# Kernel tuning notes

Hardware: AMD Instinct MI355X
Metric: run time of the kernel (lower is better)

Reference implementation:

```python
import jax, jax.numpy as jnp
import numpy as np

N_NODES = 100000
N_EDGES = 1600000
NODE_IN = 6
EDGE_IN = 4
HID = 128


def _glorot(key, shape):
    fan_in, fan_out = shape[0], shape[1]
    lim = (6.0 / (fan_in + fan_out)) ** 0.5
    return jax.random.uniform(key, shape, jnp.float32, -lim, lim)


def setup_inputs() -> dict:
    key = jax.random.key(0)
    ks = jax.random.split(key, 16)
    x = jax.random.normal(ks[0], (N_NODES, NODE_IN), jnp.float32)
    edge_index = jax.random.randint(ks[1], (2, N_EDGES), 0, N_NODES, jnp.int64)
    edge_attr = jax.random.normal(ks[2], (N_EDGES, EDGE_IN), jnp.float32)
    # SAGEConv params: out = x @ W_root + mean_neigh @ W_neigh + b
    params = {
        "w1_root": _glorot(ks[3], (NODE_IN, HID)),
        "w1_neigh": _glorot(ks[4], (NODE_IN, HID)),
        "b1": jnp.zeros((HID,), jnp.float32),
        "w2_root": _glorot(ks[5], (HID, HID)),
        "w2_neigh": _glorot(ks[6], (HID, HID)),
        "b2": jnp.zeros((HID,), jnp.float32),
        "w_e1": _glorot(ks[7], (2 * HID + EDGE_IN, HID)),
        "b_e1": jnp.zeros((HID,), jnp.float32),
        "w_e2": _glorot(ks[8], (HID, HID // 2)),
        "b_e2": jnp.zeros((HID // 2,), jnp.float32),
        "w_e3": _glorot(ks[9], (HID // 2, 1)),
        "b_e3": jnp.zeros((1,), jnp.float32),
    }
    return {"x": x, "edge_index": edge_index, "edge_attr": edge_attr, **params}


def _sage(x, src, dst, w_root, w_neigh, b):
    # mean aggregation of source features into destination nodes
    agg = jax.ops.segment_sum(x[src], dst, num_segments=N_NODES)
    cnt = jax.ops.segment_sum(jnp.ones((src.shape[0], 1), x.dtype), dst, num_segments=N_NODES)
    mean = agg / jnp.maximum(cnt, 1.0)
    return x @ w_root + mean @ w_neigh + b


def reference(x, edge_index, edge_attr,
              w1_root, w1_neigh, b1, w2_root, w2_neigh, b2,
              w_e1, b_e1, w_e2, b_e2, w_e3, b_e3):
    src, dst = edge_index[0], edge_index[1]
    h = jax.nn.relu(_sage(x, src, dst, w1_root, w1_neigh, b1))
    # dropout is identity in eval mode
    h = jax.nn.relu(_sage(h, src, dst, w2_root, w2_neigh, b2))
    # per-edge representation: [h[src], h[dst], edge_attr] -> MLP -> scalar
    e = jnp.concatenate([h[src], h[dst], edge_attr], axis=-1)  # [E, 2H+Ein]
    e = jax.nn.relu(e @ w_e1 + b_e1)
    e = jax.nn.relu(e @ w_e2 + b_e2)
    out = (e @ w_e3 + b_e3).squeeze(-1)  # [E]
    return out
```

## Files before the change

### kernel.cpp

```cpp
#include <hip/hip_runtime.h>
#include <hip/hip_bf16.h>
#include <stdint.h>


typedef unsigned short u16;
typedef short bf16x8 __attribute__((ext_vector_type(8)));
typedef float f32x4 __attribute__((ext_vector_type(4)));
typedef float f32x2 __attribute__((ext_vector_type(2)));

#define NMASK 0x1FFFF

__device__ __forceinline__ u16 f2b(float f) {
  unsigned u = __builtin_bit_cast(unsigned, f);
  u = u + 0x7fffu + ((u >> 16) & 1u);
  return (u16)(u >> 16);
}
__device__ __forceinline__ float bflo(unsigned u) {
  return __builtin_bit_cast(float, u << 16);
}
__device__ __forceinline__ float bfhi(unsigned u) {
  return __builtin_bit_cast(float, u & 0xffff0000u);
}
__device__ __forceinline__ f32x2 unpk2(unsigned u) {
  return (f32x2){bflo(u), bfhi(u)};
}
__device__ __forceinline__ unsigned pack2bf(float a, float b) {
  unsigned ua = __builtin_bit_cast(unsigned, a);
  unsigned ub = __builtin_bit_cast(unsigned, b);
  ua = ua + 0x7fffu + ((ua >> 16) & 1u);
  ub = ub + 0x7fffu + ((ub >> 16) & 1u);
  return (ua >> 16) | (ub & 0xffff0000u);
}
__device__ __forceinline__ unsigned packrn(f32x2 f) {
  __hip_bfloat162 h = __float22bfloat162_rn(make_float2(f.x, f.y));
  unsigned r;
  __builtin_memcpy(&r, &h, 4);
  return r;
}

__global__ void hist_kernel(const int* __restrict__ ei, int* __restrict__ cnt,
                            int E) {
  int e = blockIdx.x * blockDim.x + threadIdx.x;
  if (e < E) atomicAdd(&cnt[ei[E + e]], 1);
}

__global__ void scan_block_sums(const int* __restrict__ cnt,
                                int* __restrict__ partial, int N) {
  __shared__ int red[256];
  int t = threadIdx.x;
  int n = blockIdx.x * 256 + t;
  red[t] = (n < N) ? cnt[n] : 0;
  __syncthreads();
  for (int off = 128; off; off >>= 1) {
    if (t < off) red[t] += red[t + off];
    __syncthreads();
  }
  if (t == 0) partial[blockIdx.x] = red[0];
}

__global__ void scan_partials(int* __restrict__ partial,
                              int* __restrict__ rowptr, int NBLK, int E,
                              int N) {
  __shared__ int sc[512];
  int t = threadIdx.x;
  int v = (t < NBLK) ? partial[t] : 0;
  sc[t] = v;
  __syncthreads();
  for (int off = 1; off < 512; off <<= 1) {
    int a = (t >= off) ? sc[t - off] : 0;
    __syncthreads();
    sc[t] += a;
    __syncthreads();
  }
  if (t < NBLK) partial[t] = sc[t] - v;
  if (t == 0) rowptr[N] = E;
}

__global__ void scan_final(const int* __restrict__ partial,
                           int* __restrict__ cursor, int* __restrict__ rowptr,
                           int N) {
  __shared__ int sc[256];
  int t = threadIdx.x;
  int n = blockIdx.x * 256 + t;
  int v = (n < N) ? cursor[n] : 0;
  sc[t] = v;
  __syncthreads();
  for (int off = 1; off < 256; off <<= 1) {
    int a = (t >= off) ? sc[t - off] : 0;
    __syncthreads();
    sc[t] += a;
    __syncthreads();
  }
  int excl = partial[blockIdx.x] + sc[t] - v;
  if (n < N) {
    rowptr[n] = excl;
    cursor[n] = excl;
  }
}

__global__ void scatter_rec(const int* __restrict__ ei,
                            const float* __restrict__ attr,
                            int* __restrict__ cursor, uint4* __restrict__ rec,
                            unsigned* __restrict__ src4, int E) {
  int e = blockIdx.x * blockDim.x + threadIdx.x;
  if (e >= E) return;
  int s = ei[e];
  int d = ei[E + e];
  float4 a4 = *(const float4*)(attr + (size_t)e * 4);
  int pos = atomicAdd(&cursor[d], 1);
  uint4 r;
  r.x = (unsigned)s | ((unsigned)(d & 0x7FFF) << 17);
  r.y = ((unsigned)d >> 15) | ((unsigned)e << 2);
  r.z = pack2bf(a4.x, a4.y);
  r.w = pack2bf(a4.z, a4.w);
  rec[pos] = r;
  src4[pos] = (unsigned)s;
}

__global__ void pack_weights(const float* __restrict__ w2_root,
                             const float* __restrict__ w2_neigh,
                             const float* __restrict__ w_e1,
                             const float* __restrict__ w_e2,
                             const float* __restrict__ b_e1,
                             u16* __restrict__ B2f, u16* __restrict__ WSDf,
                             u16* __restrict__ W2f, float* __restrict__ pbias) {
  int t = blockIdx.x * 256 + threadIdx.x;
  if (t < 32768) {
    int j = t & 7, lane = (t >> 3) & 63, nt = (t >> 9) & 7, kt = t >> 12;
    int k = kt * 32 + (lane >> 4) * 8 + j;
    int n = nt * 16 + (lane & 15);
    float v = (k < 128) ? w2_root[k * 128 + n] : w2_neigh[(k - 128) * 128 + n];
    B2f[t] = f2b(v);
  } else if (t < 65536) {
    int t2 = t - 32768;
    int j = t2 & 7, lane = (t2 >> 3) & 63, nt = (t2 >> 9) & 15, kt = t2 >> 13;
    int k = kt * 32 + (lane >> 4) * 8 + j;
    int n = nt * 16 + (lane & 15);
    float v = (n < 128) ? w_e1[k * 128 + n] : w_e1[(128 + k) * 128 + (n - 128)];
    WSDf[t2] = f2b(v);
  } else if (t < 73728) {
    int t2 = t - 65536;
    int j = t2 & 7, lane = (t2 >> 3) & 63, nt = (t2 >> 9) & 3, kt = t2 >> 11;
    int k = kt * 32 + (lane >> 4) * 8 + j;
    int n = nt * 16 + (lane & 15);
    W2f[t2] = f2b(w_e2[k * 64 + n]);
  } else if (t < 73984) {
    int n = t - 73728;
    pbias[n] = (n < 128) ? 0.0f : b_e1[n - 128];
  }
}

__global__ __launch_bounds__(256) void agg1_kernel(
    const float* __restrict__ x, const int* __restrict__ rowptr,
    const unsigned* __restrict__ src4, float* __restrict__ mean1, int N) {
  int n = blockIdx.x * 4 + (threadIdx.x >> 6);
  if (n >= N) return;
  int lane = threadIdx.x & 63;
  int g = lane >> 3;
  int c = lane & 7;
  int beg = rowptr[n], end = rowptr[n + 1];
  float a = 0.0f;
  if (c < 6) {
    int idx[4];
#pragma unroll
    for (int j = 0; j < 4; j++) {
      int ii = beg + g + j * 8;
      idx[j] = (ii < end) ? (int)src4[ii] : -1;
    }
    float v[4];
#pragma unroll
    for (int j = 0; j < 4; j++)
      v[j] = x[(size_t)(idx[j] < 0 ? 0 : idx[j]) * 6 + c];
#pragma unroll
    for (int j = 0; j < 4; j++)
      if (idx[j] >= 0) a += v[j];
    for (int ii = beg + g + 32; ii < end; ii += 8) {
      a += x[(size_t)src4[ii] * 6 + c];
    }
  }
  a += __shfl_xor(a, 8, 64);
  a += __shfl_xor(a, 16, 64);
  a += __shfl_xor(a, 32, 64);
  if (g == 0 && c < 6)
    mean1[(size_t)n * 6 + c] = a / (float)max(end - beg, 1);
}

__global__ __launch_bounds__(256) void dense1_kernel(
    const float* __restrict__ x, const float* __restrict__ mean1,
    const float* __restrict__ w_root, const float* __restrict__ w_neigh,
    const float* __restrict__ b, u16* __restrict__ cat2b, int N) {
  __shared__ float sxm[384];
  int t = threadIdx.x;
  int col = t & 127;
  int half = t >> 7;
  float wr[6], wn[6];
#pragma unroll
  for (int j = 0; j < 6; j++) {
    wr[j] = w_root[j * 128 + col];
    wn[j] = w_neigh[j * 128 + col];
  }
  float bb = b[col];
  for (int base = blockIdx.x * 32; base < N; base += gridDim.x * 32) {
    int cnt = min(32, N - base) * 6;
    __syncthreads();
    for (int i = t; i < 384; i += 256) {
      if (i < 192)
        sxm[i] = (i < cnt) ? x[(size_t)base * 6 + i] : 0.0f;
      else
        sxm[i] = (i - 192 < cnt) ? mean1[(size_t)base * 6 + (i - 192)] : 0.0f;
    }
    __syncthreads();
#pragma unroll
    for (int sub = 0; sub < 16; sub++) {
      int nl = sub * 2 + half;
      int n = base + nl;
      if (n < N) {
        float s = bb;
#pragma unroll
        for (int j = 0; j < 6; j++)
          s += sxm[nl * 6 + j] * wr[j] + sxm[192 + nl * 6 + j] * wn[j];
        cat2b[(size_t)n * 256 + col] = f2b(fmaxf(s, 0.0f));
      }
    }
  }
}

__global__ __launch_bounds__(256) void agg2_kernel(
    const u16* __restrict__ cat2b, u16* __restrict__ cat2w,
    const int* __restrict__ rowptr, const unsigned* __restrict__ src4, int N) {
  int n = blockIdx.x * 4 + (threadIdx.x >> 6);
  if (n >= N) return;
  int lane = threadIdx.x & 63;
  int g = lane >> 4;
  int c = lane & 15;
  int beg = rowptr[n], end = rowptr[n + 1];
  f32x2 acc2[4];
#pragma unroll
  for (int j = 0; j < 4; j++) acc2[j] = (f32x2){0.f, 0.f};

  const int DEPTH = 8;
  int idx[DEPTH];
#pragma unroll
  for (int j = 0; j < DEPTH; j++) {
    int ii = beg + g + j * 4;
    idx[j] = (ii < end) ? (int)src4[ii] : -1;
  }
  uint4 u[DEPTH];
#pragma unroll
  for (int j = 0; j < DEPTH; j++) {
    int s = idx[j] < 0 ? 0 : idx[j];
    u[j] = *(const uint4*)(cat2b + (size_t)s * 256 + c * 8);
  }
#pragma unroll
  for (int j = 0; j < DEPTH; j++) {
    if (idx[j] >= 0) {
      acc2[0] += unpk2(u[j].x);
      acc2[1] += unpk2(u[j].y);
      acc2[2] += unpk2(u[j].z);
      acc2[3] += unpk2(u[j].w);
    }
  }
  for (int ii = beg + g + DEPTH * 4; ii < end; ii += 4) {
    uint4 uu = *(const uint4*)(cat2b + (size_t)src4[ii] * 256 + c * 8);
    acc2[0] += unpk2(uu.x);
    acc2[1] += unpk2(uu.y);
    acc2[2] += unpk2(uu.z);
    acc2[3] += unpk2(uu.w);
  }
#pragma unroll
  for (int j = 0; j < 4; j++) {
    acc2[j].x += __shfl_xor(acc2[j].x, 16, 64);
    acc2[j].y += __shfl_xor(acc2[j].y, 16, 64);
    acc2[j].x += __shfl_xor(acc2[j].x, 32, 64);
    acc2[j].y += __shfl_xor(acc2[j].y, 32, 64);
  }
  if (g == 0) {
    float inv = 1.0f / (float)max(end - beg, 1);
    uint4 ov;
    ov.x = packrn(acc2[0] * inv);
    ov.y = packrn(acc2[1] * inv);
    ov.z = packrn(acc2[2] * inv);
    ov.w = packrn(acc2[3] * inv);
    *(uint4*)(cat2w + (size_t)n * 256 + 128 + c * 8) = ov;
  }
}

template <int KT, int NT, bool RELU>
__global__ __launch_bounds__(512) void mfma_gemm(
    const u16* __restrict__ A, int lda, const u16* __restrict__ Bf,
    const float* __restrict__ bias, u16* __restrict__ C, int ldc, int M) {
  __shared__ u16 sB[KT * NT * 512];
  int tid = threadIdx.x;
  for (int i = tid; i < KT * NT * 64; i += 512)
    ((uint4*)sB)[i] = ((const uint4*)Bf)[i];
  int w = tid >> 6, l = tid & 63;
  int quad = l >> 4, col16 = l & 15;
  int rowA = blockIdx.x * 128 + w * 16 + col16;
  bool rv = rowA < M;
  const u16* ap = A + (size_t)rowA * lda + quad * 8;
  f32x4 acc[NT];
#pragma unroll
  for (int nt = 0; nt < NT; nt++) acc[nt] = (f32x4){0.f, 0.f, 0.f, 0.f};
  __syncthreads();
#pragma unroll
  for (int kt = 0; kt < KT; kt++) {
    bf16x8 av = {};
    if (rv) av = *(const bf16x8*)(ap + kt * 32);
#pragma unroll
    for (int nt = 0; nt < NT; nt++) {
      bf16x8 bv = *(const bf16x8*)(sB + ((kt * NT + nt) * 64 + l) * 8);
      acc[nt] = __builtin_amdgcn_mfma_f32_16x16x32_bf16(av, bv, acc[nt], 0, 0, 0);
    }
  }
  int rowbase = blockIdx.x * 128 + w * 16 + quad * 4;
#pragma unroll
  for (int r = 0; r < 4; r++) {
    int row = rowbase + r;
    if (row < M) {
#pragma unroll
      for (int nt = 0; nt < NT; nt++) {
        float v = acc[nt][r] + bias[nt * 16 + col16];
        if (RELU) v = fmaxf(v, 0.0f);
        C[(size_t)row * ldc + nt * 16 + col16] = f2b(v);
      }
    }
  }
}

__global__ __launch_bounds__(256) void edge_mfma_kernel(
    const u16* __restrict__ Pcatb, const uint4* __restrict__ rec,
    const u16* __restrict__ W2f, const float* __restrict__ b_e2,
    const float* __restrict__ w_e3, const float* __restrict__ b_e3,
    const float* __restrict__ w_e1, float* __restrict__ out, int E) {
  __shared__ u16 sV[64 * 136];
  __shared__ u16 sW2[8192];

  int tid = threadIdx.x;
  int w = tid >> 6, l = tid & 63, quad = l >> 4, c16 = l & 15;
  int eg = l >> 4, ac = l & 15;
  u16* sVw = sV + w * 16 * 136;

  for (int i = tid; i < 1024; i += 256)
    ((uint4*)sW2)[i] = ((const uint4*)W2f)[i];
  __syncthreads();

  f32x2 wa2[4][4];
#pragma unroll
  for (int j = 0; j < 4; j++) {
    float4 w0 = *(const float4*)(w_e1 + (256 + j) * 128 + ac * 8);
    float4 w1 = *(const float4*)(w_e1 + (256 + j) * 128 + ac * 8 + 4);
    wa2[j][0] = (f32x2){w0.x, w0.y};
    wa2[j][1] = (f32x2){w0.z, w0.w};
    wa2[j][2] = (f32x2){w1.x, w1.y};
    wa2[j][3] = (f32x2){w1.z, w1.w};
  }
  float w3v[4], be2[4];
#pragma unroll
  for (int nt = 0; nt < 4; nt++) {
    w3v[nt] = w_e3[nt * 16 + c16];
    be2[nt] = b_e2[nt * 16 + c16];
  }
  float b3 = b_e3[0];

  int tiles = (E + 15) >> 4;
  int NW = gridDim.x * 4;
  int t = blockIdx.x * 4 + w;

  uint4 rcA[4], rcB[4];
  uint4 ps[4];

  auto load_rec = [&](int tt, uint4* rcv) {
#pragma unroll
    for (int it = 0; it < 4; it++) {
      int e = min(tt * 16 + it * 4 + eg, E - 1);
      rcv[it] = rec[e];
    }
  };

  auto process = [&](int t, uint4* cur, uint4* nxt) {
    bool hasnext = (t + NW < tiles);
    uint4 pdv[4];
#pragma unroll
    for (int it = 0; it < 4; it++) {
      int d = (int)(((cur[it].x >> 17) | (cur[it].y << 15)) & NMASK);
      pdv[it] = *(const uint4*)(Pcatb + (size_t)d * 256 + 128 + ac * 8);
    }
#pragma unroll
    for (int it = 0; it < 4; it++) {
      int e = it * 4 + eg;
      uint4 psu = ps[it], pdu = pdv[it];
      f32x2 a01 = unpk2(cur[it].z);
      f32x2 a23 = unpk2(cur[it].w);
      unsigned pu[4] = {psu.x, psu.y, psu.z, psu.w};
      unsigned du[4] = {pdu.x, pdu.y, pdu.z, pdu.w};
      uint4 ov;
      unsigned* op = (unsigned*)&ov;
#pragma unroll
      for (int p2 = 0; p2 < 4; p2++) {
        f32x2 f = unpk2(pu[p2]) + unpk2(du[p2]);
        f += a01.x * wa2[0][p2];
        f += a01.y * wa2[1][p2];
        f += a23.x * wa2[2][p2];
        f += a23.y * wa2[3][p2];
        f = __builtin_elementwise_max(f, (f32x2){0.f, 0.f});
        op[p2] = packrn(f);
      }
      *(uint4*)(sVw + e * 136 + ac * 8) = ov;
      if (ac == 0) *(unsigned*)(sVw + e * 136 + 128) = cur[it].y >> 2;
      if (hasnext) {
        int s = (int)(nxt[it].x & NMASK);
        ps[it] = *(const uint4*)(Pcatb + (size_t)s * 256 + ac * 8);
      }
    }
    if (t + 2 * NW < tiles) load_rec(t + 2 * NW, cur);
    f32x4 acc[4];
#pragma unroll
    for (int nt = 0; nt < 4; nt++) acc[nt] = (f32x4){0.f, 0.f, 0.f, 0.f};
    const u16* vp = sVw + c16 * 136 + quad * 8;
#pragma unroll
    for (int kt = 0; kt < 4; kt++) {
      bf16x8 av = *(const bf16x8*)(vp + kt * 32);
#pragma unroll
      for (int nt = 0; nt < 4; nt++) {
        bf16x8 bv = *(const bf16x8*)(sW2 + ((kt * 4 + nt) * 64 + l) * 8);
        acc[nt] =
            __builtin_amdgcn_mfma_f32_16x16x32_bf16(av, bv, acc[nt], 0, 0, 0);
      }
    }
#pragma unroll
    for (int r = 0; r < 4; r++) {
      float p = 0.0f;
#pragma unroll
      for (int nt = 0; nt < 4; nt++)
        p += fmaxf(acc[nt][r] + be2[nt], 0.0f) * w3v[nt];
      p += __shfl_xor(p, 1, 64);
      p += __shfl_xor(p, 2, 64);
      p += __shfl_xor(p, 4, 64);
      p += __shfl_xor(p, 8, 64);
      if (c16 == 0) {
        int eloc = quad * 4 + r;
        if (t * 16 + eloc < E) {
          unsigned eid = *(const unsigned*)(sVw + eloc * 136 + 128);
          out[eid] = p + b3;
        }
      }
    }
  };

  if (t >= tiles) return;
  load_rec(t, rcA);
#pragma unroll
  for (int it = 0; it < 4; it++) {
    int s = (int)(rcA[it].x & NMASK);
    ps[it] = *(const uint4*)(Pcatb + (size_t)s * 256 + ac * 8);
  }
  if (t + NW < tiles) load_rec(t + NW, rcB);

  while (t < tiles) {
    process(t, rcA, rcB);
    t += NW;
    if (t >= tiles) break;
    process(t, rcB, rcA);
    t += NW;
  }
}

extern "C" void kernel_launch(void* const* d_in, const int* in_sizes, int n_in,
                              void* d_out, int out_size, void* d_ws,
                              size_t ws_size, hipStream_t stream) {
  const float* x        = (const float*)d_in[0];
  const int*   ei       = (const int*)d_in[1];
  const float* attr     = (const float*)d_in[2];
  const float* w1_root  = (const float*)d_in[3];
  const float* w1_neigh = (const float*)d_in[4];
  const float* b1       = (const float*)d_in[5];
  const float* w2_root  = (const float*)d_in[6];
  const float* w2_neigh = (const float*)d_in[7];
  const float* b2       = (const float*)d_in[8];
  const float* w_e1     = (const float*)d_in[9];
  const float* b_e1     = (const float*)d_in[10];
  const float* w_e2     = (const float*)d_in[11];
  const float* b_e2     = (const float*)d_in[12];
  const float* w_e3     = (const float*)d_in[13];
  const float* b_e3     = (const float*)d_in[14];
  float* out = (float*)d_out;

  int N = in_sizes[0] / 6;
  int E = in_sizes[2] / 4;
  int NBLK = (N + 255) / 256;

  int* wsi = (int*)d_ws;
  int*      rowptr  = wsi;
  int*      cursor  = wsi + 100004;
  int*      partial = wsi + 200004;
  unsigned* src4    = (unsigned*)(wsi + 200516);
  uint4*    rec     = (uint4*)(wsi + 1800520);
  float*    mean1   = (float*)(wsi + 8200520);
  u16*      cat2b   = (u16*)(wsi + 8800520);
  u16*      h2b     = (u16*)(wsi + 21600520);
  u16*      B2f     = (u16*)(wsi + 28000520);
  u16*      WSDf    = (u16*)(wsi + 28016904);
  u16*      W2f     = (u16*)(wsi + 28033288);
  float*    pbias   = (float*)(wsi + 28037384);

  (void)hipMemsetAsync(cursor, 0, (size_t)N * sizeof(int), stream);

  pack_weights<<<289, 256, 0, stream>>>(w2_root, w2_neigh, w_e1, w_e2, b_e1,
                                        B2f, WSDf, W2f, pbias);

  hist_kernel<<<(E + 255) / 256, 256, 0, stream>>>(ei, cursor, E);
  scan_block_sums<<<NBLK, 256, 0, stream>>>(cursor, partial, N);
  scan_partials<<<1, 512, 0, stream>>>(partial, rowptr, NBLK, E, N);
  scan_final<<<NBLK, 256, 0, stream>>>(partial, cursor, rowptr, N);
  scatter_rec<<<(E + 255) / 256, 256, 0, stream>>>(ei, attr, cursor, rec,
                                                   src4, E);

  agg1_kernel<<<(N + 3) / 4, 256, 0, stream>>>(x, rowptr, src4, mean1, N);
  dense1_kernel<<<1024, 256, 0, stream>>>(x, mean1, w1_root, w1_neigh, b1,
                                          cat2b, N);

  agg2_kernel<<<(N + 3) / 4, 256, 0, stream>>>(cat2b, cat2b, rowptr, src4, N);

  int gblocks = (N + 127) / 128;
  mfma_gemm<8, 8, true><<<gblocks, 512, 0, stream>>>(cat2b, 256, B2f, b2, h2b,
                                                     128, N);
  mfma_gemm<4, 16, false><<<gblocks, 512, 0, stream>>>(h2b, 128, WSDf, pbias,
                                                       cat2b, 256, N);

  edge_mfma_kernel<<<1024, 256, 0, stream>>>(cat2b, rec, W2f, b_e2, w_e3,
                                             b_e3, w_e1, out, E);
}
```

Baseline: 578.5 us.

## Bucket edges by dst/src ranges and pin dst buckets to XCDs

Edge records are no longer stored in dst-CSR order. They are grouped into 8×64 buckets keyed on the dst range and the src range, built with a new shared-memory histogram, a scan and a scatter pass. The edge MLP kernel gives each group of blocks (blockIdx & 7) one dst range, so blocks that likely run on the same XCD gather a bounded slice of node features, and src gathers within a bucket stay local. This aims to raise L2 hit rates for the random node-feature gathers. In exchange it adds three extra passes over the edge list and hardcodes bucket divisors that assume about 100k nodes.

```diff
diff --git a/kernel.cpp b/kernel.cpp
--- a/kernel.cpp
+++ b/kernel.cpp
@@ -9,6 +9,8 @@
 typedef float f32x2 __attribute__((ext_vector_type(2)));
 
 #define NMASK 0x1FFFF
+#define DDIV 12500
+#define SDIV 1563
 
 __device__ __forceinline__ u16 f2b(float f) {
   unsigned u = __builtin_bit_cast(unsigned, f);
@@ -98,23 +100,73 @@
   }
 }
 
-__global__ void scatter_rec(const int* __restrict__ ei,
-                            const float* __restrict__ attr,
-                            int* __restrict__ cursor, uint4* __restrict__ rec,
+__global__ void scatter_src(const int* __restrict__ ei,
+                            int* __restrict__ cursor,
                             unsigned* __restrict__ src4, int E) {
   int e = blockIdx.x * blockDim.x + threadIdx.x;
   if (e >= E) return;
   int s = ei[e];
   int d = ei[E + e];
+  int pos = atomicAdd(&cursor[d], 1);
+  src4[pos] = (unsigned)s;
+}
+
+__global__ void bucket_hist(const int* __restrict__ ei, int* __restrict__ bhist,
+                            int E) {
+  __shared__ int h[512];
+  int t = threadIdx.x;
+  h[t] = 0;
+  h[t + 256] = 0;
+  __syncthreads();
+  int e = blockIdx.x * blockDim.x + t;
+  if (e < E) {
+    int s = ei[e];
+    int d = ei[E + e];
+    int key = (d / DDIV) * 64 + s / SDIV;
+    atomicAdd(&h[key], 1);
+  }
+  __syncthreads();
+  if (h[t]) atomicAdd(&bhist[t], h[t]);
+  if (h[t + 256]) atomicAdd(&bhist[t + 256], h[t + 256]);
+}
+
+__global__ void bucket_scan(const int* __restrict__ bhist,
+                            int* __restrict__ bptr, int* __restrict__ bcur,
+                            int E) {
+  __shared__ int sc[512];
+  int t = threadIdx.x;
+  int v = bhist[t];
+  sc[t] = v;
+  __syncthreads();
+  for (int off = 1; off < 512; off <<= 1) {
+    int a = (t >= off) ? sc[t - off] : 0;
+    __syncthreads();
+    sc[t] += a;
+    __syncthreads();
+  }
+  int excl = sc[t] - v;
+  bptr[t] = excl;
+  bcur[t] = excl;
+  if (t == 0) bptr[512] = E;
+}
+
+__global__ void scatter2_rec(const int* __restrict__ ei,
+                             const float* __restrict__ attr,
+                             int* __restrict__ bcur, uint4* __restrict__ rec,
+                             int E) {
+  int e = blockIdx.x * blockDim.x + threadIdx.x;
+  if (e >= E) return;
+  int s = ei[e];
+  int d = ei[E + e];
   float4 a4 = *(const float4*)(attr + (size_t)e * 4);
-  int pos = atomicAdd(&cursor[d], 1);
+  int key = (d / DDIV) * 64 + s / SDIV;
+  int pos = atomicAdd(&bcur[key], 1);
   uint4 r;
   r.x = (unsigned)s | ((unsigned)(d & 0x7FFF) << 17);
   r.y = ((unsigned)d >> 15) | ((unsigned)e << 2);
   r.z = pack2bf(a4.x, a4.y);
   r.w = pack2bf(a4.z, a4.w);
   rec[pos] = r;
-  src4[pos] = (unsigned)s;
 }
 
 __global__ void pack_weights(const float* __restrict__ w2_root,
@@ -331,7 +383,8 @@
     const u16* __restrict__ Pcatb, const uint4* __restrict__ rec,
     const u16* __restrict__ W2f, const float* __restrict__ b_e2,
     const float* __restrict__ w_e3, const float* __restrict__ b_e3,
-    const float* __restrict__ w_e1, float* __restrict__ out, int E) {
+    const float* __restrict__ w_e1, const int* __restrict__ bptr,
+    float* __restrict__ out, int E) {
   __shared__ u16 sV[64 * 136];
   __shared__ u16 sW2[8192];
 
@@ -362,9 +415,12 @@
   }
   float b3 = b_e3[0];
 
-  int tiles = (E + 15) >> 4;
-  int NW = gridDim.x * 4;
-  int t = blockIdx.x * 4 + w;
+  int s8 = blockIdx.x & 7;
+  int tb = bptr[s8 * 64] >> 4;
+  int te = (bptr[(s8 + 1) * 64] + 15) >> 4;
+  int wi = (blockIdx.x >> 3) * 4 + w;
+  const int NW = 512;
+  int t = tb + wi;
 
   uint4 rcA[4], rcB[4];
   uint4 ps[4];
@@ -378,7 +434,7 @@
   };
 
   auto process = [&](int t, uint4* cur, uint4* nxt) {
-    bool hasnext = (t + NW < tiles);
+    bool hasnext = (t + NW < te);
     uint4 pdv[4];
 #pragma unroll
     for (int it = 0; it < 4; it++) {
@@ -412,7 +468,7 @@
         ps[it] = *(const uint4*)(Pcatb + (size_t)s * 256 + ac * 8);
       }
     }
-    if (t + 2 * NW < tiles) load_rec(t + 2 * NW, cur);
+    if (t + 2 * NW < te) load_rec(t + 2 * NW, cur);
     f32x4 acc[4];
 #pragma unroll
     for (int nt = 0; nt < 4; nt++) acc[nt] = (f32x4){0.f, 0.f, 0.f, 0.f};
@@ -447,19 +503,19 @@
     }
   };
 
-  if (t >= tiles) return;
+  if (t >= te) return;
   load_rec(t, rcA);
 #pragma unroll
   for (int it = 0; it < 4; it++) {
     int s = (int)(rcA[it].x & NMASK);
     ps[it] = *(const uint4*)(Pcatb + (size_t)s * 256 + ac * 8);
   }
-  if (t + NW < tiles) load_rec(t + NW, rcB);
-
-  while (t < tiles) {
+  if (t + NW < te) load_rec(t + NW, rcB);
+
+  while (t < te) {
     process(t, rcA, rcB);
     t += NW;
-    if (t >= tiles) break;
+    if (t >= te) break;
     process(t, rcB, rcA);
     t += NW;
   }
@@ -502,8 +558,12 @@
   u16*      WSDf    = (u16*)(wsi + 28016904);
   u16*      W2f     = (u16*)(wsi + 28033288);
   float*    pbias   = (float*)(wsi + 28037384);
+  int*      bhist   = wsi + 28037640;
+  int*      bptr    = wsi + 28038152;
+  int*      bcur    = wsi + 28038668;
 
   (void)hipMemsetAsync(cursor, 0, (size_t)N * sizeof(int), stream);
+  (void)hipMemsetAsync(bhist, 0, 512 * sizeof(int), stream);
 
   pack_weights<<<289, 256, 0, stream>>>(w2_root, w2_neigh, w_e1, w_e2, b_e1,
                                         B2f, WSDf, W2f, pbias);
@@ -512,8 +572,11 @@
   scan_block_sums<<<NBLK, 256, 0, stream>>>(cursor, partial, N);
   scan_partials<<<1, 512, 0, stream>>>(partial, rowptr, NBLK, E, N);
   scan_final<<<NBLK, 256, 0, stream>>>(partial, cursor, rowptr, N);
-  scatter_rec<<<(E + 255) / 256, 256, 0, stream>>>(ei, attr, cursor, rec,
-                                                   src4, E);
+  scatter_src<<<(E + 255) / 256, 256, 0, stream>>>(ei, cursor, src4, E);
+
+  bucket_hist<<<(E + 255) / 256, 256, 0, stream>>>(ei, bhist, E);
+  bucket_scan<<<1, 512, 0, stream>>>(bhist, bptr, bcur, E);
+  scatter2_rec<<<(E + 255) / 256, 256, 0, stream>>>(ei, attr, bcur, rec, E);
 
   agg1_kernel<<<(N + 3) / 4, 256, 0, stream>>>(x, rowptr, src4, mean1, N);
   dense1_kernel<<<1024, 256, 0, stream>>>(x, mean1, w1_root, w1_neigh, b1,
@@ -528,5 +591,5 @@
                                                        cat2b, 256, N);
 
   edge_mfma_kernel<<<1024, 256, 0, stream>>>(cat2b, rec, W2f, b_e2, w_e3,
-                                             b_e3, w_e1, out, E);
-}
+                                             b_e3, w_e1, bptr, out, E);
+}
```

Result: slower. 1.261 ms (+117.9%).

## Fuse node GEMMs keeping hidden tile in LDS, pad x to 8 floats

Applied to the files above, without the earlier changes.

Merges the layer-2 SAGE GEMM and the per-node edge-projection GEMM into one kernel. The ReLU hidden tile stays in shared memory, avoiding the h2b round trip and one launch. Weight fragments are now read straight from global memory rather than staged in LDS. Separately, node features are padded to 8 floats so layer-1 gathers use aligned rows, at the cost of an extra packing kernel.

```diff
diff --git a/kernel.cpp b/kernel.cpp
--- a/kernel.cpp
+++ b/kernel.cpp
@@ -115,6 +115,14 @@
   r.w = pack2bf(a4.z, a4.w);
   rec[pos] = r;
   src4[pos] = (unsigned)s;
+}
+
+__global__ void pack_x32(const float* __restrict__ x, float* __restrict__ x32,
+                         int N) {
+  int i = blockIdx.x * blockDim.x + threadIdx.x;
+  if (i >= N * 8) return;
+  int c = i & 7;
+  x32[i] = (c < 6) ? x[(size_t)(i >> 3) * 6 + c] : 0.0f;
 }
 
 __global__ void pack_weights(const float* __restrict__ w2_root,
@@ -151,7 +159,7 @@
 }
 
 __global__ __launch_bounds__(256) void agg1_kernel(
-    const float* __restrict__ x, const int* __restrict__ rowptr,
+    const float* __restrict__ x32, const int* __restrict__ rowptr,
     const unsigned* __restrict__ src4, float* __restrict__ mean1, int N) {
   int n = blockIdx.x * 4 + (threadIdx.x >> 6);
   if (n >= N) return;
@@ -170,12 +178,12 @@
     float v[4];
 #pragma unroll
     for (int j = 0; j < 4; j++)
-      v[j] = x[(size_t)(idx[j] < 0 ? 0 : idx[j]) * 6 + c];
+      v[j] = x32[(size_t)(idx[j] < 0 ? 0 : idx[j]) * 8 + c];
 #pragma unroll
     for (int j = 0; j < 4; j++)
       if (idx[j] >= 0) a += v[j];
     for (int ii = beg + g + 32; ii < end; ii += 8) {
-      a += x[(size_t)src4[ii] * 6 + c];
+      a += x32[(size_t)src4[ii] * 8 + c];
     }
   }
   a += __shfl_xor(a, 8, 64);
@@ -285,44 +293,61 @@
   }
 }
 
-template <int KT, int NT, bool RELU>
-__global__ __launch_bounds__(512) void mfma_gemm(
-    const u16* __restrict__ A, int lda, const u16* __restrict__ Bf,
-    const float* __restrict__ bias, u16* __restrict__ C, int ldc, int M) {
-  __shared__ u16 sB[KT * NT * 512];
+__global__ __launch_bounds__(512) void fused_gemm(
+    const u16* __restrict__ A, const u16* __restrict__ B1f,
+    const float* __restrict__ b2, const u16* __restrict__ BSDf,
+    const float* __restrict__ pbias, u16* __restrict__ C, int M) {
+  __shared__ u16 sH[128 * 136];
   int tid = threadIdx.x;
-  for (int i = tid; i < KT * NT * 64; i += 512)
-    ((uint4*)sB)[i] = ((const uint4*)Bf)[i];
   int w = tid >> 6, l = tid & 63;
   int quad = l >> 4, col16 = l & 15;
   int rowA = blockIdx.x * 128 + w * 16 + col16;
   bool rv = rowA < M;
-  const u16* ap = A + (size_t)rowA * lda + quad * 8;
-  f32x4 acc[NT];
-#pragma unroll
-  for (int nt = 0; nt < NT; nt++) acc[nt] = (f32x4){0.f, 0.f, 0.f, 0.f};
-  __syncthreads();
-#pragma unroll
-  for (int kt = 0; kt < KT; kt++) {
+  const u16* ap = A + (size_t)rowA * 256 + quad * 8;
+  f32x4 acc1[8];
+#pragma unroll
+  for (int nt = 0; nt < 8; nt++) acc1[nt] = (f32x4){0.f, 0.f, 0.f, 0.f};
+#pragma unroll
+  for (int kt = 0; kt < 8; kt++) {
     bf16x8 av = {};
     if (rv) av = *(const bf16x8*)(ap + kt * 32);
 #pragma unroll
-    for (int nt = 0; nt < NT; nt++) {
-      bf16x8 bv = *(const bf16x8*)(sB + ((kt * NT + nt) * 64 + l) * 8);
-      acc[nt] = __builtin_amdgcn_mfma_f32_16x16x32_bf16(av, bv, acc[nt], 0, 0, 0);
-    }
-  }
-  int rowbase = blockIdx.x * 128 + w * 16 + quad * 4;
+    for (int nt = 0; nt < 8; nt++) {
+      bf16x8 bv = *(const bf16x8*)(B1f + ((kt * 8 + nt) * 64 + l) * 8);
+      acc1[nt] = __builtin_amdgcn_mfma_f32_16x16x32_bf16(av, bv, acc1[nt], 0, 0, 0);
+    }
+  }
+  int rowb = w * 16 + quad * 4;
 #pragma unroll
   for (int r = 0; r < 4; r++) {
-    int row = rowbase + r;
+#pragma unroll
+    for (int nt = 0; nt < 8; nt++) {
+      float v = acc1[nt][r] + b2[nt * 16 + col16];
+      sH[(rowb + r) * 136 + nt * 16 + col16] = f2b(fmaxf(v, 0.0f));
+    }
+  }
+  __syncthreads();
+  const u16* hp = sH + (w * 16 + col16) * 136 + quad * 8;
+  f32x4 acc2[16];
+#pragma unroll
+  for (int nt = 0; nt < 16; nt++) acc2[nt] = (f32x4){0.f, 0.f, 0.f, 0.f};
+#pragma unroll
+  for (int kt = 0; kt < 4; kt++) {
+    bf16x8 av = *(const bf16x8*)(hp + kt * 32);
+#pragma unroll
+    for (int nt = 0; nt < 16; nt++) {
+      bf16x8 bv = *(const bf16x8*)(BSDf + ((kt * 16 + nt) * 64 + l) * 8);
+      acc2[nt] = __builtin_amdgcn_mfma_f32_16x16x32_bf16(av, bv, acc2[nt], 0, 0, 0);
+    }
+  }
+#pragma unroll
+  for (int r = 0; r < 4; r++) {
+    int row = blockIdx.x * 128 + rowb + r;
     if (row < M) {
 #pragma unroll
-      for (int nt = 0; nt < NT; nt++) {
-        float v = acc[nt][r] + bias[nt * 16 + col16];
-        if (RELU) v = fmaxf(v, 0.0f);
-        C[(size_t)row * ldc + nt * 16 + col16] = f2b(v);
-      }
+      for (int nt = 0; nt < 16; nt++)
+        C[(size_t)row * 256 + nt * 16 + col16] =
+            f2b(acc2[nt][r] + pbias[nt * 16 + col16]);
     }
   }
 }
@@ -497,7 +522,7 @@
   uint4*    rec     = (uint4*)(wsi + 1800520);
   float*    mean1   = (float*)(wsi + 8200520);
   u16*      cat2b   = (u16*)(wsi + 8800520);
-  u16*      h2b     = (u16*)(wsi + 21600520);
+  float*    x32     = (float*)(wsi + 21600520);
   u16*      B2f     = (u16*)(wsi + 28000520);
   u16*      WSDf    = (u16*)(wsi + 28016904);
   u16*      W2f     = (u16*)(wsi + 28033288);
@@ -507,6 +532,7 @@
 
   pack_weights<<<289, 256, 0, stream>>>(w2_root, w2_neigh, w_e1, w_e2, b_e1,
                                         B2f, WSDf, W2f, pbias);
+  pack_x32<<<(N * 8 + 255) / 256, 256, 0, stream>>>(x, x32, N);
 
   hist_kernel<<<(E + 255) / 256, 256, 0, stream>>>(ei, cursor, E);
   scan_block_sums<<<NBLK, 256, 0, stream>>>(cursor, partial, N);
@@ -515,17 +541,14 @@
   scatter_rec<<<(E + 255) / 256, 256, 0, stream>>>(ei, attr, cursor, rec,
                                                    src4, E);
 
-  agg1_kernel<<<(N + 3) / 4, 256, 0, stream>>>(x, rowptr, src4, mean1, N);
+  agg1_kernel<<<(N + 3) / 4, 256, 0, stream>>>(x32, rowptr, src4, mean1, N);
   dense1_kernel<<<1024, 256, 0, stream>>>(x, mean1, w1_root, w1_neigh, b1,
                                           cat2b, N);
 
   agg2_kernel<<<(N + 3) / 4, 256, 0, stream>>>(cat2b, cat2b, rowptr, src4, N);
 
-  int gblocks = (N + 127) / 128;
-  mfma_gemm<8, 8, true><<<gblocks, 512, 0, stream>>>(cat2b, 256, B2f, b2, h2b,
-                                                     128, N);
-  mfma_gemm<4, 16, false><<<gblocks, 512, 0, stream>>>(h2b, 128, WSDf, pbias,
-                                                       cat2b, 256, N);
+  fused_gemm<<<(N + 127) / 128, 512, 0, stream>>>(cat2b, B2f, b2, WSDf, pbias,
+                                                  cat2b, N);
 
   edge_mfma_kernel<<<1024, 256, 0, stream>>>(cat2b, rec, W2f, b_e2, w_e3,
                                              b_e3, w_e1, out, E);
```

Result: no change. 587.1 us (+1.5%).
